# Optimization experiments

Measured on AMD Instinct MI355X. Metric: run time of the kernel, lower is better.

The kernel has to match this reference:

```python
import jax, jax.numpy as jnp
import numpy as np

RESO = 32
PADDING = 0.02


def setup_inputs() -> dict:
    key = jax.random.key(0)
    ks = jax.random.split(key, 8)
    N, P, F, H, C = 8, 131072, 32, 128, 32
    return {
        "points": jax.random.uniform(ks[0], (N, P, 3), dtype=jnp.float32),
        "feature": jax.random.normal(ks[1], (N, P, F), dtype=jnp.float32),
        "fc0_w": jax.random.normal(ks[2], (F, F), dtype=jnp.float32) / np.sqrt(F),
        "fc0_b": jnp.zeros((F,), jnp.float32),
        "fc1_w": jax.random.normal(ks[3], (F, H), dtype=jnp.float32) / np.sqrt(F),
        "fc1_b": jnp.zeros((H,), jnp.float32),
        "sc_w": jax.random.normal(ks[4], (F, H), dtype=jnp.float32) / np.sqrt(F),
        "conv_w": jax.random.normal(ks[5], (C, H), dtype=jnp.float32) / np.sqrt(H),
        "conv_b": jnp.zeros((C,), jnp.float32),
    }


def _coord_to_index(points):
    # pad_and_crop_coordinate3d: shrink unit cube by padding, clip into [0,1)
    q = (points - 0.5) / (1.0 + PADDING + 1e-3) + 0.5
    q = jnp.clip(q, 0.0, 1.0 - 1e-6)
    xyz = (q * RESO).astype(jnp.int32)  # [N,P,3]
    idx = xyz[..., 0] + RESO * (xyz[..., 1] + RESO * xyz[..., 2])  # [N,P]
    return idx


def reference(points, feature, fc0_w, fc0_b, fc1_w, fc1_b, sc_w, conv_w, conv_b):
    N, P, _ = feature.shape
    H = fc1_w.shape[1]
    R3 = RESO ** 3

    idx = _coord_to_index(points)  # [N,P] int32

    # ResnetBlockFC: shortcut(x) + fc1(relu(fc0(relu(x))))
    a = jax.nn.relu(feature)
    net = jax.nn.relu(a @ fc0_w + fc0_b)
    h = feature @ sc_w + (net @ fc1_w + fc1_b)  # [N,P,H]

    # scatter_max into voxel bins (empty bins -> 0, torch_scatter convention)
    seg = (idx + jnp.arange(N, dtype=jnp.int32)[:, None] * R3).reshape(-1)
    pooled = jax.ops.segment_max(h.reshape(N * P, H), seg, num_segments=N * R3)
    pooled = jnp.where(jnp.isneginf(pooled), 0.0, pooled)
    grid = pooled.reshape(N, R3, H)  # [N,R3,H]

    # 1x1x1 Conv3d == per-voxel channel mix
    out = jnp.einsum('nvh,ch->nvc', grid, conv_w) + conv_b
    feature_grid = out.transpose(0, 2, 1).reshape(N, -1, RESO, RESO, RESO)
    index = idx[:, None, :]  # [N,1,P]
    return index, feature_grid
```

## Files before the change

kernel.cpp:

```cpp
#include <hip/hip_runtime.h>

#define RESO 32
#define R3   32768
#define NB   8
#define PP   131072
#define FF   32
#define HH   128
#define CC   32
#define CAP  64
#define NPTS (NB*PP)
#define NSEG (NB*R3)

typedef __attribute__((ext_vector_type(8))) __bf16 bf16x8;
typedef __attribute__((ext_vector_type(4))) float  f32x4;

__device__ __forceinline__ f32x4 MFMA(bf16x8 a, bf16x8 b, f32x4 c) {
    return __builtin_amdgcn_mfma_f32_16x16x32_bf16(a, b, c, 0, 0, 0);
}

__global__ __launch_bounds__(256) void lpbe_bin(
    const float* __restrict__ points,
    unsigned* __restrict__ count,
    unsigned* __restrict__ bucket,
    float* __restrict__ index_out)
{
    int gid = blockIdx.x * 256 + threadIdx.x;

    const float* pp = points + (size_t)gid * 3;
    float px = pp[0], py = pp[1], pz = pp[2];
    const float DIV = 1.021f;
    const float HIq = (float)(1.0 - 1e-6);
    float qx = (px - 0.5f)/DIV + 0.5f; qx = fminf(fmaxf(qx, 0.0f), HIq);
    float qy = (py - 0.5f)/DIV + 0.5f; qy = fminf(fmaxf(qy, 0.0f), HIq);
    float qz = (pz - 0.5f)/DIV + 0.5f; qz = fminf(fmaxf(qz, 0.0f), HIq);
    int xi = (int)(qx * 32.0f);
    int yi = (int)(qy * 32.0f);
    int zi = (int)(qz * 32.0f);
    int idx = xi + RESO*(yi + RESO*zi);

    index_out[gid] = (float)idx;

    int seg = (gid >> 17) * R3 + idx;
    unsigned slot = atomicAdd(&count[seg], 1u);
    if (slot < CAP) bucket[(size_t)seg * CAP + slot] = (unsigned)gid;
}

__global__ __launch_bounds__(256, 3) void lpbe_pool(
    const float* __restrict__ feature,
    const float* __restrict__ fc0_w, const float* __restrict__ fc0_b,
    const float* __restrict__ fc1_w, const float* __restrict__ fc1_b,
    const float* __restrict__ sc_w,
    const float* __restrict__ conv_w, const float* __restrict__ conv_b,
    const unsigned* __restrict__ count, const unsigned* __restrict__ bucket,
    float* __restrict__ out)
{
    __shared__ __bf16 s_bsc[8][64*8];
    __shared__ __bf16 s_bw1[8][64*8];
    __shared__ __bf16 s_w0f[2][64*8];
    __shared__ __bf16 s_cwf[8][64*8];
    __shared__ __bf16 s_net [4][16*40];
    __shared__ __bf16 s_pool[4][16*136];

    const int tid  = threadIdx.x;
    const int wv   = tid >> 6;
    const int lane = tid & 63;
    const int c16  = lane & 15;
    const int g    = lane >> 4;

    for (int nt = wv; nt < 8; nt += 4) {
        bf16x8 v, w;
        #pragma unroll
        for (int e = 0; e < 8; ++e) {
            int k = 8*g + e;
            v[e] = (__bf16)sc_w [k*HH + 16*nt + c16];
            w[e] = (__bf16)fc1_w[k*HH + 16*nt + c16];
        }
        *(bf16x8*)&s_bsc[nt][lane*8] = v;
        *(bf16x8*)&s_bw1[nt][lane*8] = w;
    }
    if (wv < 2) {
        bf16x8 v;
        #pragma unroll
        for (int e = 0; e < 8; ++e)
            v[e] = (__bf16)fc0_w[(8*g + e)*FF + 16*wv + c16];
        *(bf16x8*)&s_w0f[wv][lane*8] = v;
    }
    for (int fi = wv; fi < 8; fi += 4) {
        int ch = fi >> 2, kk = fi & 3;
        bf16x8 v;
        #pragma unroll
        for (int e = 0; e < 8; ++e)
            v[e] = (__bf16)conv_w[(16*ch + c16)*HH + 32*kk + 8*g + e];
        *(bf16x8*)&s_cwf[fi][lane*8] = v;
    }

    const float b0v0 = fc0_b[c16], b0v1 = fc0_b[16 + c16];
    float b1v[8];
    #pragma unroll
    for (int nt = 0; nt < 8; ++nt) b1v[nt] = fc1_b[16*nt + c16];
    const float cb0 = conv_b[c16], cb1 = conv_b[16 + c16];
    __syncthreads();

    const int wgid = blockIdx.x * 4 + wv;
    const int tb16 = wgid * 16;
    __bf16* snet  = s_net[wv];
    __bf16* spool = s_pool[wv];

    int cntv = (int)count[tb16 + c16];
    if (cntv > CAP) cntv = CAP;

    unsigned pid0 = 0, pid1 = 0;
    int kA0 = 0, kB0 = 0, kA1 = 0, kB1 = 0;
    f32x4 fa0, fb0, fa1, fb1;

#define LOADP(PIDX, S) do {                                                  \
    int _Pv = (PIDX);                                                        \
    kA##S = __builtin_amdgcn_readlane(cntv, 2*_Pv);                          \
    kB##S = __builtin_amdgcn_readlane(cntv, 2*_Pv + 1);                      \
    unsigned _pid = bucket[(size_t)(tb16 + 2*_Pv + (c16 >> 3))*CAP           \
                           + (c16 & 7)];                                     \
    pid##S = _pid & (NPTS - 1);                       \
} while (0)

#define LOADF(S) do {                                                        \
    const float* _fp = feature + (size_t)pid##S * FF + 8*g;                  \
    fa##S = *(const f32x4*)_fp;                                              \
    fb##S = *(const f32x4*)(_fp + 4);                                        \
} while (0)

#define STEP(Q, S, SN) do {                                                  \
    const int _q = (Q);                                                      \
    const int _kA = kA##S, _kB = kB##S;                                      \
    if (_q < 6) LOADP(_q + 2, S);                     \
    if (_q < 7) LOADF(SN);                        \
    float run[8];                                                            \
    _Pragma("unroll")                                                        \
    for (int nt = 0; nt < 8; ++nt) run[nt] = -3.0e38f;                       \
    int _km = _kA > _kB ? _kA : _kB;                                         \
    int _T  = (_km + 7) >> 3;                                                \
    for (int t = 0; t < _T; ++t) {                                           \
        f32x4 u0, u1;                                                        \
        if (t == 0) { u0 = fa##S; u1 = fb##S; }                              \
        else {                                                               \
            unsigned _pid = bucket[(size_t)(tb16 + 2*_q + (c16 >> 3))*CAP    \
                                   + 8*t + (c16 & 7)] & (NPTS - 1);          \
            const float* _fp = feature + (size_t)_pid * FF + 8*g;            \
            u0 = *(const f32x4*)_fp;                                         \
            u1 = *(const f32x4*)(_fp + 4);                                   \
        }                                                                    \
        bf16x8 ar, aw;                                                       \
        _Pragma("unroll")                                                    \
        for (int e = 0; e < 4; ++e) {                                        \
            ar[e]   = (__bf16)u0[e];            ar[4+e] = (__bf16)u1[e];     \
            aw[e]   = (__bf16)fmaxf(u0[e],0.f); aw[4+e] = (__bf16)fmaxf(u1[e],0.f); \
        }                                                                    \
        bf16x8 w00 = *(const bf16x8*)&s_w0f[0][lane*8];                      \
        bf16x8 w01 = *(const bf16x8*)&s_w0f[1][lane*8];                      \
        f32x4 n0 = {0.f,0.f,0.f,0.f}, n1 = {0.f,0.f,0.f,0.f};                \
        n0 = MFMA(aw, w00, n0);                                              \
        n1 = MFMA(aw, w01, n1);                                              \
        _Pragma("unroll")                                                    \
        for (int r = 0; r < 4; ++r) {                                        \
            snet[(4*g + r)*40 + c16]      = (__bf16)fmaxf(n0[r] + b0v0, 0.f);\
            snet[(4*g + r)*40 + 16 + c16] = (__bf16)fmaxf(n1[r] + b0v1, 0.f);\
        }                                                                    \
        asm volatile("s_waitcnt lgkmcnt(0)" ::: "memory");                   \
        bf16x8 an = *(const bf16x8*)&snet[c16*40 + 8*g];                     \
        f32x4 mv;                                                            \
        _Pragma("unroll")                                                    \
        for (int r = 0; r < 4; ++r) {                                        \
            int _sl = 8*t + 4*(g & 1) + r;                                   \
            mv[r] = (_sl < ((g < 2) ? _kA : _kB)) ? 0.f : -3.0e38f;          \
        }                                                                    \
        _Pragma("unroll")                                                    \
        for (int nt = 0; nt < 8; ++nt) {                                     \
            bf16x8 bs = *(const bf16x8*)&s_bsc[nt][lane*8];                  \
            bf16x8 bw = *(const bf16x8*)&s_bw1[nt][lane*8];                  \
            f32x4 acc = mv;                                                  \
            acc = MFMA(ar, bs, acc);                                         \
            acc = MFMA(an, bw, acc);                                         \
            run[nt] = fmaxf(run[nt],                                         \
                      fmaxf(fmaxf(acc[0],acc[1]), fmaxf(acc[2],acc[3])));    \
        }                                                                    \
    }                                                                        \
    _Pragma("unroll")                                                        \
    for (int nt = 0; nt < 8; ++nt) {                                         \
        float m = fmaxf(run[nt], __shfl_xor(run[nt], 16));                   \
        float sel = (((g < 2) ? _kA : _kB) == 0) ? 0.f : (m + b1v[nt]);      \
        if (g == 0)      spool[(2*_q  )*136 + 16*nt + c16] = (__bf16)sel;    \
        else if (g == 2) spool[(2*_q+1)*136 + 16*nt + c16] = (__bf16)sel;    \
    }                                                                        \
} while (0)

    LOADP(0, 0);
    LOADF(0);
    LOADP(1, 1);

    #pragma unroll
    for (int m = 0; m < 4; ++m) {
        STEP(2*m,     0, 1);
        STEP(2*m + 1, 1, 0);
    }

    asm volatile("s_waitcnt lgkmcnt(0)" ::: "memory");
    f32x4 o0 = {cb0, cb0, cb0, cb0};
    f32x4 o1 = {cb1, cb1, cb1, cb1};
    #pragma unroll
    for (int kk = 0; kk < 4; ++kk) {
        bf16x8 ap  = *(const bf16x8*)&spool[c16*136 + 32*kk + 8*g];
        bf16x8 bc0 = *(const bf16x8*)&s_cwf[kk    ][lane*8];
        bf16x8 bc1 = *(const bf16x8*)&s_cwf[4 + kk][lane*8];
        o0 = MFMA(ap, bc0, o0);
        o1 = MFMA(ap, bc1, o1);
    }
    const int n  = tb16 >> 15;
    const int vb = tb16 & (R3 - 1);
    float* ob = out + (size_t)n*CC*R3 + (size_t)vb + 4*g;
    *(f32x4*)(ob + (size_t)c16*R3)        = o0;
    *(f32x4*)(ob + (size_t)(16 + c16)*R3) = o1;

#undef STEP
#undef LOADF
#undef LOADP
}

extern "C" void kernel_launch(void* const* d_in, const int* in_sizes, int n_in,
                              void* d_out, int out_size, void* d_ws, size_t ws_size,
                              hipStream_t stream)
{
    const float* points  = (const float*)d_in[0];
    const float* feature = (const float*)d_in[1];
    const float* fc0_w   = (const float*)d_in[2];
    const float* fc0_b   = (const float*)d_in[3];
    const float* fc1_w   = (const float*)d_in[4];
    const float* fc1_b   = (const float*)d_in[5];
    const float* sc_w    = (const float*)d_in[6];
    const float* conv_w  = (const float*)d_in[7];
    const float* conv_b  = (const float*)d_in[8];

    unsigned* count  = (unsigned*)d_ws;
    unsigned* bucket = count + NSEG;
    float* out0 = (float*)d_out;
    float* out1 = out0 + (size_t)NPTS;

    hipMemsetAsync(count, 0, (size_t)NSEG * sizeof(unsigned), stream);
    lpbe_bin <<<NPTS/256, 256, 0, stream>>>(points, count, bucket, out0);
    lpbe_pool<<<NSEG/64,  256, 0, stream>>>(feature, fc0_w, fc0_b, fc1_w, fc1_b,
                                            sc_w, conv_w, conv_b, count, bucket, out1);
}
```

Before: 182.2 us.

## Keep fc0 output in registers via transposed MFMA and drop LDS round-trip

The fc0 MFMA now runs with swapped operands so its output lands in the layout the next MFMA expects as its A operand. The fc1 weights are stored in LDS with a permuted K order to match, which removes the per-step LDS store, wait and reload of the hidden activations. The conv weights are loaded straight from global into registers at the end instead of being staged in LDS. Together with the smaller LDS footprint, the occupancy hint rises from 3 to 4 blocks, at the cost of more register pressure.

Result: slower. 283.1 us (+55.4%).

```diff
diff --git a/kernel.cpp b/kernel.cpp
--- a/kernel.cpp
+++ b/kernel.cpp
@@ -45,7 +45,7 @@
     if (slot < CAP) bucket[(size_t)seg * CAP + slot] = (unsigned)gid;
 }
 
-__global__ __launch_bounds__(256, 3) void lpbe_pool(
+__global__ __launch_bounds__(256, 4) void lpbe_pool(
     const float* __restrict__ feature,
     const float* __restrict__ fc0_w, const float* __restrict__ fc0_b,
     const float* __restrict__ fc1_w, const float* __restrict__ fc1_b,
@@ -57,8 +57,6 @@
     __shared__ __bf16 s_bsc[8][64*8];
     __shared__ __bf16 s_bw1[8][64*8];
     __shared__ __bf16 s_w0f[2][64*8];
-    __shared__ __bf16 s_cwf[8][64*8];
-    __shared__ __bf16 s_net [4][16*40];
     __shared__ __bf16 s_pool[4][16*136];
 
     const int tid  = threadIdx.x;
@@ -71,9 +69,10 @@
         bf16x8 v, w;
         #pragma unroll
         for (int e = 0; e < 8; ++e) {
-            int k = 8*g + e;
-            v[e] = (__bf16)sc_w [k*HH + 16*nt + c16];
-            w[e] = (__bf16)fc1_w[k*HH + 16*nt + c16];
+            int kn = 8*g + e;
+            int ks = (e < 4) ? (4*g + e) : (16 + 4*g + e-4);
+            v[e] = (__bf16)sc_w [kn*HH + 16*nt + c16];
+            w[e] = (__bf16)fc1_w[ks*HH + 16*nt + c16];
         }
         *(bf16x8*)&s_bsc[nt][lane*8] = v;
         *(bf16x8*)&s_bw1[nt][lane*8] = w;
@@ -85,16 +84,9 @@
             v[e] = (__bf16)fc0_w[(8*g + e)*FF + 16*wv + c16];
         *(bf16x8*)&s_w0f[wv][lane*8] = v;
     }
-    for (int fi = wv; fi < 8; fi += 4) {
-        int ch = fi >> 2, kk = fi & 3;
-        bf16x8 v;
-        #pragma unroll
-        for (int e = 0; e < 8; ++e)
-            v[e] = (__bf16)conv_w[(16*ch + c16)*HH + 32*kk + 8*g + e];
-        *(bf16x8*)&s_cwf[fi][lane*8] = v;
-    }
-
-    const float b0v0 = fc0_b[c16], b0v1 = fc0_b[16 + c16];
+
+    const f32x4 b0A = *(const f32x4*)&fc0_b[4*g];
+    const f32x4 b0B = *(const f32x4*)&fc0_b[16 + 4*g];
     float b1v[8];
     #pragma unroll
     for (int nt = 0; nt < 8; ++nt) b1v[nt] = fc1_b[16*nt + c16];
@@ -103,7 +95,6 @@
 
     const int wgid = blockIdx.x * 4 + wv;
     const int tb16 = wgid * 16;
-    __bf16* snet  = s_net[wv];
     __bf16* spool = s_pool[wv];
 
     int cntv = (int)count[tb16 + c16];
@@ -156,16 +147,15 @@
         }                                                                    \
         bf16x8 w00 = *(const bf16x8*)&s_w0f[0][lane*8];                      \
         bf16x8 w01 = *(const bf16x8*)&s_w0f[1][lane*8];                      \
-        f32x4 n0 = {0.f,0.f,0.f,0.f}, n1 = {0.f,0.f,0.f,0.f};                \
-        n0 = MFMA(aw, w00, n0);                                              \
-        n1 = MFMA(aw, w01, n1);                                              \
+        f32x4 zz = {0.f,0.f,0.f,0.f};                                        \
+        f32x4 n0 = MFMA(w00, aw, zz);          \
+        f32x4 n1 = MFMA(w01, aw, zz);         \
+        bf16x8 an;                             \
         _Pragma("unroll")                                                    \
         for (int r = 0; r < 4; ++r) {                                        \
-            snet[(4*g + r)*40 + c16]      = (__bf16)fmaxf(n0[r] + b0v0, 0.f);\
-            snet[(4*g + r)*40 + 16 + c16] = (__bf16)fmaxf(n1[r] + b0v1, 0.f);\
-        }                                                                    \
-        asm volatile("s_waitcnt lgkmcnt(0)" ::: "memory");                   \
-        bf16x8 an = *(const bf16x8*)&snet[c16*40 + 8*g];                     \
+            an[r]   = (__bf16)fmaxf(n0[r] + b0A[r], 0.f);                    \
+            an[4+r] = (__bf16)fmaxf(n1[r] + b0B[r], 0.f);                    \
+        }                                                                    \
         f32x4 mv;                                                            \
         _Pragma("unroll")                                                    \
         for (int r = 0; r < 4; ++r) {                                        \
@@ -202,16 +192,27 @@
         STEP(2*m + 1, 1, 0);
     }
 
+    bf16x8 cw0[4], cw1[4];
+    #pragma unroll
+    for (int kk = 0; kk < 4; ++kk) {
+        f32x4 a0 = *(const f32x4*)&conv_w[(size_t)c16*HH        + 32*kk + 8*g];
+        f32x4 a1 = *(const f32x4*)&conv_w[(size_t)c16*HH        + 32*kk + 8*g + 4];
+        f32x4 c0 = *(const f32x4*)&conv_w[(size_t)(16+c16)*HH   + 32*kk + 8*g];
+        f32x4 c1 = *(const f32x4*)&conv_w[(size_t)(16+c16)*HH   + 32*kk + 8*g + 4];
+        #pragma unroll
+        for (int e = 0; e < 4; ++e) {
+            cw0[kk][e] = (__bf16)a0[e]; cw0[kk][4+e] = (__bf16)a1[e];
+            cw1[kk][e] = (__bf16)c0[e]; cw1[kk][4+e] = (__bf16)c1[e];
+        }
+    }
     asm volatile("s_waitcnt lgkmcnt(0)" ::: "memory");
     f32x4 o0 = {cb0, cb0, cb0, cb0};
     f32x4 o1 = {cb1, cb1, cb1, cb1};
     #pragma unroll
     for (int kk = 0; kk < 4; ++kk) {
-        bf16x8 ap  = *(const bf16x8*)&spool[c16*136 + 32*kk + 8*g];
-        bf16x8 bc0 = *(const bf16x8*)&s_cwf[kk    ][lane*8];
-        bf16x8 bc1 = *(const bf16x8*)&s_cwf[4 + kk][lane*8];
-        o0 = MFMA(ap, bc0, o0);
-        o1 = MFMA(ap, bc1, o1);
+        bf16x8 ap = *(const bf16x8*)&spool[c16*136 + 32*kk + 8*g];
+        o0 = MFMA(ap, cw0[kk], o0);
+        o1 = MFMA(ap, cw1[kk], o1);
     }
     const int n  = tb16 >> 15;
     const int vb = tb16 & (R3 - 1);
```
